# Performance work log

Hardware: AMD Instinct MI355X
Metric: run time of the kernel (lower is better)

The kernel has to match this reference:

```python
import jax, jax.numpy as jnp
import numpy as np

IN_SIZE = 1024
OUT_SIZE = 4096
RANK = 4
NSTACK = (OUT_SIZE + IN_SIZE - 1) // IN_SIZE  # 4


def setup_inputs() -> dict:
    key = jax.random.key(0)
    k1, k2, k3, k4 = jax.random.split(key, 4)
    init_std = float(np.sqrt(1.0 / (RANK * IN_SIZE)))
    x = jax.random.normal(k1, (2, 2048, IN_SIZE), dtype=jnp.float32)
    G = jax.random.normal(k2, (NSTACK, RANK, IN_SIZE), dtype=jnp.float32) * init_std
    H = jax.random.normal(k3, (NSTACK, RANK, IN_SIZE), dtype=jnp.float32) * init_std
    bound = 1.0 / float(np.sqrt(IN_SIZE))
    bias = jax.random.uniform(k4, (OUT_SIZE,), dtype=jnp.float32, minval=-bound, maxval=bound)
    return {"x": x, "G": G, "H": H, "bias": bias}


def reference(x, G, H, bias):
    n = x.shape[-1]
    nstack, rank, _ = G.shape
    out_size = bias.shape[0]
    u = x.reshape(-1, n)                     # (B, n) flattened tokens
    # Stage 1: circular conv of reversed input with H filters (zero-padded to 2n)
    u_f = jnp.fft.rfft(u[:, ::-1], n=2 * n, axis=-1)        # (B, n+1) complex
    H_f = jnp.fft.rfft(H, n=2 * n, axis=-1)                 # (nstack, rank, n+1)
    uv_f = u_f[:, None, None, :] * H_f                       # (B, nstack, rank, n+1)
    # irfft(..., 2n)[..., reverse_idx] == first n samples reversed
    tr = jnp.fft.irfft(uv_f, n=2 * n, axis=-1)[..., :n][..., ::-1]  # (B, nstack, rank, n)
    # Stage 2: conv with G filters, summed over rank
    w_f = jnp.fft.rfft(tr, n=2 * n, axis=-1)                # (B, nstack, rank, n+1)
    G_f = jnp.fft.rfft(G, n=2 * n, axis=-1)                 # (nstack, rank, n+1)
    wv_sum_f = jnp.einsum('bsrf,srf->bsf', w_f, G_f)        # sum over rank
    out = jnp.fft.irfft(wv_sum_f, n=2 * n, axis=-1)[..., :n]  # (B, nstack, n)
    out = out.reshape(u.shape[0], nstack * n)[:, :out_size] + bias
    return out.reshape(x.shape[:-1] + (out_size,))
```

## Files before the change

kernel.cpp:

```cpp
#include <hip/hip_runtime.h>
#include <hip/hip_bf16.h>

#define NIN 1024
#define NOUT 4096
#define NTOK 4096
#define NSTACK 4
#define RANK 4

typedef __bf16 bf16x8 __attribute__((ext_vector_type(8)));
typedef float f32x4 __attribute__((ext_vector_type(4)));

__global__ __launch_bounds__(256) void prep_kernel(const float* __restrict__ x,
                                                   const float* __restrict__ G,
                                                   const float* __restrict__ H,
                                                   __bf16* __restrict__ xb,
                                                   __bf16* __restrict__ M) {
  int bid = blockIdx.x;
  if (bid < 2048) {
    int i = (bid * 256 + threadIdx.x) * 8;
    float4 a = *reinterpret_cast<const float4*>(x + i);
    float4 b = *reinterpret_cast<const float4*>(x + i + 4);
    bf16x8 o;
    o[0] = (__bf16)a.x; o[1] = (__bf16)a.y; o[2] = (__bf16)a.z; o[3] = (__bf16)a.w;
    o[4] = (__bf16)b.x; o[5] = (__bf16)b.y; o[6] = (__bf16)b.z; o[7] = (__bf16)b.w;
    *reinterpret_cast<bf16x8*>(xb + i) = o;
    return;
  }
  bid -= 2048;
  const int ndiag = 2 * NIN - 1;
  int wid = bid * 4 + (threadIdx.x >> 6);
  if (wid >= NSTACK * ndiag) return;
  int lane = threadIdx.x & 63;
  int s = wid / ndiag;
  int dd = wid % ndiag;
  int d = dd - (NIN - 1);
  int ad = d < 0 ? -d : d;
  int L = NIN - ad;
  int gofs = d < 0 ? -d : 0;
  int hofs = d > 0 ? d : 0;
  const float* Gs = G + s * (RANK * NIN);
  const float* Hs = H + s * (RANK * NIN);
  __bf16* Ms = M + (size_t)s * NIN * NIN;

  float carry = 0.f;
  for (int r0 = 0; r0 < L; r0 += 64) {
    int k = r0 + lane;
    float e = 0.f;
    if (k < L) {
      int gi = k + gofs, hi2 = k + hofs;
      e = Gs[gi] * Hs[hi2]
        + Gs[NIN + gi] * Hs[NIN + hi2]
        + Gs[2 * NIN + gi] * Hs[2 * NIN + hi2]
        + Gs[3 * NIN + gi] * Hs[3 * NIN + hi2];
    }
    float v = e;
    #pragma unroll
    for (int off = 1; off < 64; off <<= 1) {
      float o = __shfl_up(v, off, 64);
      if (lane >= off) v += o;
    }
    if (k < L) Ms[(size_t)(k + gofs) * NIN + (k + hofs)] = (__bf16)(carry + v);
    carry += __shfl(v, 63, 64);
  }
}

#define BM 256
#define BN 256
#define BK 32
#define ABY (BM * BK * 2)
#define BUFBY (2 * ABY)
#define KT (NIN / BK)

__device__ __forceinline__ void gload16(const char* gsrc, char* lds) {
  __builtin_amdgcn_global_load_lds(
      (const __attribute__((address_space(1))) unsigned int*)gsrc,
      (__attribute__((address_space(3))) unsigned int*)lds, 16, 0, 0);
}

#define MEMF asm volatile("" ::: "memory")
__device__ __forceinline__ void wgbar() {
  MEMF; __builtin_amdgcn_s_barrier(); MEMF;
}

__global__ __launch_bounds__(512, 2) void gemm_kernel(
    const __bf16* __restrict__ A,
    const __bf16* __restrict__ B,
    const float* __restrict__ bias,
    float* __restrict__ C) {
  __shared__ __align__(16) char smem[3 * BUFBY];

  const int tid = threadIdx.x;
  const int lane = tid & 63;
  const int lo = lane & 15;
  const int hi = lane >> 4;
  const int wid = tid >> 6;
  const int wr = wid >> 2;
  const int wc = wid & 3;

  const int orig = blockIdx.x;
  const int wg = (orig & 7) * 32 + (orig >> 3);
  const int bx = wg & 15;
  const int by = wg >> 4;
  const int brow = by * BM;
  const int bcol = bx * BN;

  const char* Ab = (const char*)(A + (size_t)brow * NIN);
  const char* Bb = (const char*)(B + (size_t)bcol * NIN);
  size_t ag[2], bg[2];
  int al[2], bl[2];
  #pragma unroll
  for (int l = 0; l < 2; ++l) {
    int P = (l * 512 + tid) * 16;
    int row = P >> 6;
    int inner = (P & 63) ^ (((row >> 1) & 3) << 4);
    al[l] = P;
    ag[l] = (size_t)row * (NIN * 2) + inner;
    bl[l] = P;
    bg[l] = (size_t)row * (NIN * 2) + inner;
  }

  const int kso = ((hi ^ ((lo >> 1) & 3)) << 4);
  const int abase = (wr * 128 + lo) * 64 + kso;
  const int bbase = ABY + (wc * 64 + lo) * 64 + kso;

  f32x4 acc[8][4];
  #pragma unroll
  for (int i = 0; i < 8; ++i)
    #pragma unroll
    for (int j = 0; j < 4; ++j)
      acc[i][j] = (f32x4){0.f, 0.f, 0.f, 0.f};

  #pragma unroll
  for (int l = 0; l < 2; ++l) gload16(Ab + ag[l], smem + al[l]);
  #pragma unroll
  for (int l = 0; l < 2; ++l) gload16(Bb + bg[l], smem + ABY + bl[l]);
  #pragma unroll
  for (int l = 0; l < 2; ++l) gload16(Ab + 64 + ag[l], smem + BUFBY + al[l]);
  #pragma unroll
  for (int l = 0; l < 2; ++l) gload16(Bb + 64 + bg[l], smem + BUFBY + ABY + bl[l]);
  asm volatile("s_waitcnt vmcnt(4)" ::: "memory");
  wgbar();

  int cb = 0;
  int sb = 2 * BUFBY;
  #pragma unroll 1
  for (int kt = 0; kt < KT; ++kt) {
    const char* buf = smem + cb;
    const int kg = (kt + 2) * 64;
    const bool dost = (kt + 2) < KT;

    bf16x8 af[4], bfr[4];
    #pragma unroll
    for (int mi = 0; mi < 4; ++mi)
      af[mi] = *(const bf16x8*)(buf + abase + mi * 1024);
    #pragma unroll
    for (int ni = 0; ni < 4; ++ni)
      bfr[ni] = *(const bf16x8*)(buf + bbase + ni * 1024);
    if (dost) {
      gload16(Ab + kg + ag[0], smem + sb + al[0]);
      gload16(Ab + kg + ag[1], smem + sb + al[1]);
    }
    wgbar();
    __builtin_amdgcn_s_setprio(1);
    #pragma unroll
    for (int mi = 0; mi < 4; ++mi)
      #pragma unroll
      for (int ni = 0; ni < 4; ++ni)
        acc[mi][ni] = __builtin_amdgcn_mfma_f32_16x16x32_bf16(af[mi], bfr[ni], acc[mi][ni], 0, 0, 0);
    __builtin_amdgcn_s_setprio(0);
    wgbar();

    bf16x8 af2[4];
    #pragma unroll
    for (int mi = 0; mi < 4; ++mi)
      af2[mi] = *(const bf16x8*)(buf + abase + (mi + 4) * 1024);
    if (dost) {
      gload16(Bb + kg + bg[0], smem + sb + ABY + bl[0]);
      gload16(Bb + kg + bg[1], smem + sb + ABY + bl[1]);
    }
    if (kt < KT - 2) asm volatile("s_waitcnt vmcnt(4)" ::: "memory");
    else             asm volatile("s_waitcnt vmcnt(0)" ::: "memory");
    wgbar();
    __builtin_amdgcn_s_setprio(1);
    #pragma unroll
    for (int mi = 0; mi < 4; ++mi)
      #pragma unroll
      for (int ni = 0; ni < 4; ++ni)
        acc[mi + 4][ni] = __builtin_amdgcn_mfma_f32_16x16x32_bf16(af2[mi], bfr[ni], acc[mi + 4][ni], 0, 0, 0);
    __builtin_amdgcn_s_setprio(0);
    wgbar();

    cb += BUFBY; if (cb == 3 * BUFBY) cb = 0;
    sb += BUFBY; if (sb == 3 * BUFBY) sb = 0;
  }

  #pragma unroll
  for (int ni = 0; ni < 4; ++ni) {
    const int col = bcol + wc * 64 + ni * 16 + lo;
    const float bv = bias[col];
    #pragma unroll
    for (int mi = 0; mi < 8; ++mi) {
      const int row0 = brow + wr * 128 + mi * 16 + hi * 4;
      float* Cp = C + (size_t)row0 * NOUT + col;
      Cp[0]                  = acc[mi][ni][0] + bv;
      Cp[(size_t)NOUT]       = acc[mi][ni][1] + bv;
      Cp[2 * (size_t)NOUT]   = acc[mi][ni][2] + bv;
      Cp[3 * (size_t)NOUT]   = acc[mi][ni][3] + bv;
    }
  }
}

extern "C" void kernel_launch(void* const* d_in, const int* in_sizes, int n_in,
                              void* d_out, int out_size, void* d_ws, size_t ws_size,
                              hipStream_t stream) {
  const float* x = (const float*)d_in[0];
  const float* G = (const float*)d_in[1];
  const float* H = (const float*)d_in[2];
  const float* bias = (const float*)d_in[3];
  float* out = (float*)d_out;

  __bf16* xb = (__bf16*)d_ws;
  __bf16* Mb = (__bf16*)((char*)d_ws + (size_t)NTOK * NIN * 2);

  prep_kernel<<<2048 + 2047, 256, 0, stream>>>(x, G, H, xb, Mb);
  gemm_kernel<<<256, 512, 0, stream>>>(xb, Mb, bias, out);
}
```

Baseline: 145.8 us.

## Restructure Toeplitz matrix build and use 4-buffer single-barrier GEMM pipeline

The prep kernel now builds the structured matrix M with lane-per-diagonal sequential accumulation in 32 blocks. This replaces one wave per diagonal doing a shuffle prefix scan over 2047*4 waves, and the matrix-build blocks are placed first so they start early. The GEMM switches from a triple-buffered LDS ring with four barriers per k-step to a quadruple-buffered ring with one wait plus barrier per step. That cuts synchronisation cost but uses more LDS and may lower occupancy. The new prep path runs long serial loops (up to 1024 iterations) in only 32 blocks, which risks a long tail, and its strided stores to M are poorly coalesced.

```diff
diff --git a/kernel.cpp b/kernel.cpp
--- a/kernel.cpp
+++ b/kernel.cpp
@@ -16,8 +16,8 @@
                                                    __bf16* __restrict__ xb,
                                                    __bf16* __restrict__ M) {
   int bid = blockIdx.x;
-  if (bid < 2048) {
-    int i = (bid * 256 + threadIdx.x) * 8;
+  if (bid >= 32) {
+    int i = ((bid - 32) * 256 + threadIdx.x) * 8;
     float4 a = *reinterpret_cast<const float4*>(x + i);
     float4 b = *reinterpret_cast<const float4*>(x + i + 4);
     bf16x8 o;
@@ -26,60 +26,56 @@
     *reinterpret_cast<bf16x8*>(xb + i) = o;
     return;
   }
-  bid -= 2048;
-  const int ndiag = 2 * NIN - 1;
-  int wid = bid * 4 + (threadIdx.x >> 6);
-  if (wid >= NSTACK * ndiag) return;
-  int lane = threadIdx.x & 63;
-  int s = wid / ndiag;
-  int dd = wid % ndiag;
-  int d = dd - (NIN - 1);
-  int ad = d < 0 ? -d : d;
-  int L = NIN - ad;
-  int gofs = d < 0 ? -d : 0;
-  int hofs = d > 0 ? d : 0;
+  const int s = bid >> 3;
+  const int band = (bid & 7) * 4 + (threadIdx.x >> 6);
+  const int lane = threadIdx.x & 63;
   const float* Gs = G + s * (RANK * NIN);
   const float* Hs = H + s * (RANK * NIN);
   __bf16* Ms = M + (size_t)s * NIN * NIN;
 
-  float carry = 0.f;
-  for (int r0 = 0; r0 < L; r0 += 64) {
-    int k = r0 + lane;
-    float e = 0.f;
-    if (k < L) {
-      int gi = k + gofs, hi2 = k + hofs;
-      e = Gs[gi] * Hs[hi2]
-        + Gs[NIN + gi] * Hs[NIN + hi2]
-        + Gs[2 * NIN + gi] * Hs[2 * NIN + hi2]
-        + Gs[3 * NIN + gi] * Hs[3 * NIN + hi2];
-    }
-    float v = e;
-    #pragma unroll
-    for (int off = 1; off < 64; off <<= 1) {
-      float o = __shfl_up(v, off, 64);
-      if (lane >= off) v += o;
-    }
-    if (k < L) Ms[(size_t)(k + gofs) * NIN + (k + hofs)] = (__bf16)(carry + v);
-    carry += __shfl(v, 63, 64);
-  }
-}
-
-#define BM 256
-#define BN 256
+  if (band < 16) {
+    const int d0 = band * 64;
+    const int myd = d0 + lane;
+    float acc = 0.f;
+    const int kmax = NIN - 1 - d0;
+    #pragma unroll 4
+    for (int k = 0; k <= kmax; ++k) {
+      const int c = k + myd;
+      const float g0 = Gs[k],           g1 = Gs[NIN + k];
+      const float g2 = Gs[2 * NIN + k], g3 = Gs[3 * NIN + k];
+      if (c <= NIN - 1) {
+        acc += g0 * Hs[c] + g1 * Hs[NIN + c] + g2 * Hs[2 * NIN + c] + g3 * Hs[3 * NIN + c];
+        Ms[(size_t)k * NIN + c] = (__bf16)acc;
+      }
+    }
+  } else {
+    const int w = band - 16;
+    const int a0 = 1 + w * 64;
+    const bool lactive = (a0 + lane) <= NIN - 1;
+    float acc = 0.f;
+    const int tmax = NIN - 1 - a0;
+    #pragma unroll 4
+    for (int tau = 0; tau <= tmax; ++tau) {
+      const int t = a0 + tau;
+      const int c = tau - lane;
+      const float g0 = Gs[t],           g1 = Gs[NIN + t];
+      const float g2 = Gs[2 * NIN + t], g3 = Gs[3 * NIN + t];
+      if (lactive && c >= 0) {
+        acc += g0 * Hs[c] + g1 * Hs[NIN + c] + g2 * Hs[2 * NIN + c] + g3 * Hs[3 * NIN + c];
+        Ms[(size_t)t * NIN + c] = (__bf16)acc;
+      }
+    }
+  }
+}
+
 #define BK 32
-#define ABY (BM * BK * 2)
-#define BUFBY (2 * ABY)
 #define KT (NIN / BK)
+#define TILEBY 32768
 
 __device__ __forceinline__ void gload16(const char* gsrc, char* lds) {
   __builtin_amdgcn_global_load_lds(
       (const __attribute__((address_space(1))) unsigned int*)gsrc,
       (__attribute__((address_space(3))) unsigned int*)lds, 16, 0, 0);
-}
-
-#define MEMF asm volatile("" ::: "memory")
-__device__ __forceinline__ void wgbar() {
-  MEMF; __builtin_amdgcn_s_barrier(); MEMF;
 }
 
 __global__ __launch_bounds__(512, 2) void gemm_kernel(
@@ -87,7 +83,7 @@
     const __bf16* __restrict__ B,
     const float* __restrict__ bias,
     float* __restrict__ C) {
-  __shared__ __align__(16) char smem[3 * BUFBY];
+  __shared__ __align__(16) char smem[4 * TILEBY];
 
   const int tid = threadIdx.x;
   const int lane = tid & 63;
@@ -101,27 +97,25 @@
   const int wg = (orig & 7) * 32 + (orig >> 3);
   const int bx = wg & 15;
   const int by = wg >> 4;
-  const int brow = by * BM;
-  const int bcol = bx * BN;
+  const int brow = by * 256;
+  const int bcol = bx * 256;
 
   const char* Ab = (const char*)(A + (size_t)brow * NIN);
   const char* Bb = (const char*)(B + (size_t)bcol * NIN);
-  size_t ag[2], bg[2];
-  int al[2], bl[2];
+  size_t gofs[2];
+  int lofs[2];
   #pragma unroll
   for (int l = 0; l < 2; ++l) {
     int P = (l * 512 + tid) * 16;
     int row = P >> 6;
     int inner = (P & 63) ^ (((row >> 1) & 3) << 4);
-    al[l] = P;
-    ag[l] = (size_t)row * (NIN * 2) + inner;
-    bl[l] = P;
-    bg[l] = (size_t)row * (NIN * 2) + inner;
+    lofs[l] = P;
+    gofs[l] = (size_t)row * (NIN * 2) + inner;
   }
 
   const int kso = ((hi ^ ((lo >> 1) & 3)) << 4);
   const int abase = (wr * 128 + lo) * 64 + kso;
-  const int bbase = ABY + (wc * 64 + lo) * 64 + kso;
+  const int bbase = 16384 + (wc * 64 + lo) * 64 + kso;
 
   f32x4 acc[8][4];
   #pragma unroll
@@ -131,24 +125,28 @@
       acc[i][j] = (f32x4){0.f, 0.f, 0.f, 0.f};
 
   #pragma unroll
-  for (int l = 0; l < 2; ++l) gload16(Ab + ag[l], smem + al[l]);
-  #pragma unroll
-  for (int l = 0; l < 2; ++l) gload16(Bb + bg[l], smem + ABY + bl[l]);
-  #pragma unroll
-  for (int l = 0; l < 2; ++l) gload16(Ab + 64 + ag[l], smem + BUFBY + al[l]);
-  #pragma unroll
-  for (int l = 0; l < 2; ++l) gload16(Bb + 64 + bg[l], smem + BUFBY + ABY + bl[l]);
-  asm volatile("s_waitcnt vmcnt(4)" ::: "memory");
-  wgbar();
-
-  int cb = 0;
-  int sb = 2 * BUFBY;
+  for (int l = 0; l < 2; ++l) gload16(Ab + gofs[l], smem + lofs[l]);
+  #pragma unroll
+  for (int l = 0; l < 2; ++l) gload16(Bb + gofs[l], smem + 16384 + lofs[l]);
+  #pragma unroll
+  for (int l = 0; l < 2; ++l) gload16(Ab + 64 + gofs[l], smem + TILEBY + lofs[l]);
+  #pragma unroll
+  for (int l = 0; l < 2; ++l) gload16(Bb + 64 + gofs[l], smem + TILEBY + 16384 + lofs[l]);
+
   #pragma unroll 1
   for (int kt = 0; kt < KT; ++kt) {
-    const char* buf = smem + cb;
+    const char* buf = smem + (kt & 3) * TILEBY;
+    char* sbuf = smem + ((kt + 2) & 3) * TILEBY;
     const int kg = (kt + 2) * 64;
     const bool dost = (kt + 2) < KT;
 
+    asm volatile("s_waitcnt vmcnt(4)" ::: "memory");
+    __builtin_amdgcn_s_barrier();
+
+    if (dost) {
+      gload16(Ab + kg + gofs[0], sbuf + lofs[0]);
+      gload16(Ab + kg + gofs[1], sbuf + lofs[1]);
+    }
     bf16x8 af[4], bfr[4];
     #pragma unroll
     for (int mi = 0; mi < 4; ++mi)
@@ -156,11 +154,6 @@
     #pragma unroll
     for (int ni = 0; ni < 4; ++ni)
       bfr[ni] = *(const bf16x8*)(buf + bbase + ni * 1024);
-    if (dost) {
-      gload16(Ab + kg + ag[0], smem + sb + al[0]);
-      gload16(Ab + kg + ag[1], smem + sb + al[1]);
-    }
-    wgbar();
     __builtin_amdgcn_s_setprio(1);
     #pragma unroll
     for (int mi = 0; mi < 4; ++mi)
@@ -168,19 +161,15 @@
       for (int ni = 0; ni < 4; ++ni)
         acc[mi][ni] = __builtin_amdgcn_mfma_f32_16x16x32_bf16(af[mi], bfr[ni], acc[mi][ni], 0, 0, 0);
     __builtin_amdgcn_s_setprio(0);
-    wgbar();
-
+
+    if (dost) {
+      gload16(Bb + kg + gofs[0], sbuf + 16384 + lofs[0]);
+      gload16(Bb + kg + gofs[1], sbuf + 16384 + lofs[1]);
+    }
     bf16x8 af2[4];
     #pragma unroll
     for (int mi = 0; mi < 4; ++mi)
       af2[mi] = *(const bf16x8*)(buf + abase + (mi + 4) * 1024);
-    if (dost) {
-      gload16(Bb + kg + bg[0], smem + sb + ABY + bl[0]);
-      gload16(Bb + kg + bg[1], smem + sb + ABY + bl[1]);
-    }
-    if (kt < KT - 2) asm volatile("s_waitcnt vmcnt(4)" ::: "memory");
-    else             asm volatile("s_waitcnt vmcnt(0)" ::: "memory");
-    wgbar();
     __builtin_amdgcn_s_setprio(1);
     #pragma unroll
     for (int mi = 0; mi < 4; ++mi)
@@ -188,10 +177,6 @@
       for (int ni = 0; ni < 4; ++ni)
         acc[mi + 4][ni] = __builtin_amdgcn_mfma_f32_16x16x32_bf16(af2[mi], bfr[ni], acc[mi + 4][ni], 0, 0, 0);
     __builtin_amdgcn_s_setprio(0);
-    wgbar();
-
-    cb += BUFBY; if (cb == 3 * BUFBY) cb = 0;
-    sb += BUFBY; if (sb == 3 * BUFBY) sb = 0;
   }
 
   #pragma unroll
@@ -202,10 +187,10 @@
     for (int mi = 0; mi < 8; ++mi) {
       const int row0 = brow + wr * 128 + mi * 16 + hi * 4;
       float* Cp = C + (size_t)row0 * NOUT + col;
-      Cp[0]                  = acc[mi][ni][0] + bv;
-      Cp[(size_t)NOUT]       = acc[mi][ni][1] + bv;
-      Cp[2 * (size_t)NOUT]   = acc[mi][ni][2] + bv;
-      Cp[3 * (size_t)NOUT]   = acc[mi][ni][3] + bv;
+      Cp[0]                = acc[mi][ni][0] + bv;
+      Cp[(size_t)NOUT]     = acc[mi][ni][1] + bv;
+      Cp[2 * (size_t)NOUT] = acc[mi][ni][2] + bv;
+      Cp[3 * (size_t)NOUT] = acc[mi][ni][3] + bv;
     }
   }
 }
@@ -222,6 +207,6 @@
   __bf16* xb = (__bf16*)d_ws;
   __bf16* Mb = (__bf16*)((char*)d_ws + (size_t)NTOK * NIN * 2);
 
-  prep_kernel<<<2048 + 2047, 256, 0, stream>>>(x, G, H, xb, Mb);
+  prep_kernel<<<32 + 2048, 256, 0, stream>>>(x, G, H, xb, Mb);
   gemm_kernel<<<256, 512, 0, stream>>>(xb, Mb, bias, out);
 }
```

After: 314.4 us. +115.6%, slower.
